# Kernel tuning notes

Hardware: AMD Instinct MI355X
Metric: run time of the kernel (lower is better)

Reference implementation:

```python
import jax, jax.numpy as jnp
import numpy as np

B, L1, L2, D1, D2, H, P = 32, 256, 64, 256, 256, 256, 128
I = D1 + D2  # gate / GRU input dim


def setup_inputs() -> dict:
    key = jax.random.key(0)
    ks = jax.random.split(key, 10)
    s = 0.05  # weight init scale
    return {
        "sequence1": jax.random.normal(ks[0], (B, L1, D1), jnp.float32),
        "sequence2": jax.random.normal(ks[1], (B, L2, D2), jnp.float32),
        "sequence1_mask": jnp.ones((B, L1), jnp.float32),
        "sequence2_mask": jnp.ones((B, L2), jnp.float32),
        "W1": jax.random.normal(ks[2], (D2, P), jnp.float32) * s,
        "W2": jax.random.normal(ks[3], (D1 + H, P), jnp.float32) * s,
        "v": jax.random.normal(ks[4], (P,), jnp.float32) * s,
        "Wg": jax.random.normal(ks[5], (I, I), jnp.float32) * s,
        "bg": jnp.zeros((I,), jnp.float32),
        "w_ih": jax.random.normal(ks[6], (3 * H, I), jnp.float32) * s,
        "w_hh": jax.random.normal(ks[7], (3 * H, H), jnp.float32) * s,
        "b_ih": jnp.zeros((3 * H,), jnp.float32),
        "b_hh": jnp.zeros((3 * H,), jnp.float32),
    }


def reference(sequence1, sequence2, sequence1_mask, sequence2_mask,
              W1, W2, v, Wg, bg, w_ih, w_hh, b_ih, b_hh):
    # Precompute sequence2 projection once: [B, L2, P]
    seq2_proj = jnp.einsum('bld,dp->blp', sequence2, W1)
    # Additive mask for softmax over L2
    neg = jnp.where(sequence2_mask > 0, 0.0, -1e9)  # [B, L2]
    xs = jnp.transpose(sequence1, (1, 0, 2))  # [L1, B, D1]

    def step(h, x_t):
        # attention: v^T tanh(W1*seq2_j + W2*[x_t; h])
        vec = jnp.concatenate([x_t, h], axis=-1)            # [B, D1+H]
        s = jnp.einsum('blp,p->bl',
                       jnp.tanh(seq2_proj + (vec @ W2)[:, None, :]), v) + neg
        w = jax.nn.softmax(s, axis=-1)                      # [B, L2]
        att = jnp.einsum('bl,bld->bd', w, sequence2)        # [B, D2]
        inp = jnp.concatenate([x_t, att], axis=-1)          # [B, I]
        # gated attention: sigmoid(Linear(inp)) * inp
        inp = jax.nn.sigmoid(inp @ Wg.T + bg) * inp
        # GRUCell (torch semantics)
        gi = inp @ w_ih.T + b_ih
        gh = h @ w_hh.T + b_hh
        ir, iz, inn = jnp.split(gi, 3, axis=-1)
        hr, hz, hn = jnp.split(gh, 3, axis=-1)
        r = jax.nn.sigmoid(ir + hr)
        z = jax.nn.sigmoid(iz + hz)
        n = jnp.tanh(inn + r * hn)
        h_new = (1.0 - z) * n + z * h
        return h_new, h_new

    h0 = jnp.zeros((sequence1.shape[0], w_hh.shape[1]), sequence1.dtype)
    _, hs = jax.lax.scan(step, h0, xs)                      # [L1, B, H]
    out = jnp.transpose(hs, (1, 0, 2)) * sequence1_mask[:, :, None]
    return out
```

## Files before the change

### kernel.cpp

```cpp
#include <hip/hip_runtime.h>

typedef _Float16 half2_v __attribute__((ext_vector_type(2)));
typedef unsigned int u32;
typedef unsigned long long u64;

#define W2K_O    0
#define WHHP_O   16384
#define WIHP_O   114688
#define NPACKW   311296
#define S2P_B    1245184
#define S2T_B    1769472
#define M1_B     2818048
#define PROJX_B  4915200
#define GATEX_B  7012352
#define EXCH_B   15400960

#define SMEM_BYTES 149648

__device__ __forceinline__ float fdot2(half2_v a, half2_v b, float c) {
    return __builtin_amdgcn_fdot2(a, b, c, false);
}
__device__ __forceinline__ half2_v h2_of(u32 u) { return __builtin_bit_cast(half2_v, u); }
__device__ __forceinline__ u32 pack_h2(float a, float b) {
    half2_v r; r[0] = (_Float16)a; r[1] = (_Float16)b;
    return __builtin_bit_cast(u32, r);
}
__device__ __forceinline__ float dot4(uint4 w, uint4 a, float acc) {
    acc = fdot2(h2_of(w.x), h2_of(a.x), acc);
    acc = fdot2(h2_of(w.y), h2_of(a.y), acc);
    acc = fdot2(h2_of(w.z), h2_of(a.z), acc);
    acc = fdot2(h2_of(w.w), h2_of(a.w), acc);
    return acc;
}
__device__ __forceinline__ float fast_tanh(float x) {
    float e = __expf(2.0f * x);
    return 1.0f - 2.0f / (e + 1.0f);
}
__device__ __forceinline__ float fast_sigmoid(float x) {
    return 1.0f / (1.0f + __expf(-x));
}
__device__ __forceinline__ u64 aload64(const u64* p) {
    return __hip_atomic_load(p, __ATOMIC_RELAXED, __HIP_MEMORY_SCOPE_AGENT);
}
__device__ __forceinline__ void astore64(u64* p, u64 v) {
    __hip_atomic_store(p, v, __ATOMIC_RELAXED, __HIP_MEMORY_SCOPE_AGENT);
}
__device__ __forceinline__ u32 mkw(float x, u32 st) {
    unsigned short hb = __builtin_bit_cast(unsigned short, (_Float16)x);
    return (st << 16) | (u32)hb;
}
__device__ __forceinline__ u64 mkw64(float a, float b, u32 st) {
    return (u64)mkw(a, st) | ((u64)mkw(b, st) << 32);
}
__device__ __forceinline__ float f16low(u32 v) {
    return (float)__builtin_bit_cast(_Float16, (unsigned short)(v & 0xFFFFu));
}

__global__ void prep_pack_w(const float* __restrict__ W2, const float* __restrict__ wih,
                            const float* __restrict__ whh, u32* __restrict__ ws_u) {
    int idx = blockIdx.x * 256 + threadIdx.x;
    if (idx >= NPACKW) return;
    float a, c;
    if (idx < WHHP_O) {
        int mm = idx >> 11, r = idx & 2047, p = r >> 4, kl = r & 15;
        int row = 256 + mm * 32 + 2 * kl;
        a = W2[row * 128 + p]; c = W2[(row + 1) * 128 + p];
    } else if (idx < WIHP_O) {
        int t2 = idx - WHHP_O, mm = t2 / 12288, r = t2 % 12288, o = r >> 7, k = r & 127;
        int row = (o >> 5) * 256 + mm * 32 + (o & 31);
        a = whh[row * 256 + 2 * k]; c = whh[row * 256 + 2 * k + 1];
    } else {
        int t2 = idx - WIHP_O, mm = t2 / 24576, r = t2 % 24576, o = r >> 8, k = r & 255;
        int row = (o >> 5) * 256 + mm * 32 + (o & 31);
        a = wih[row * 512 + 2 * k]; c = wih[row * 512 + 2 * k + 1];
    }
    ws_u[idx] = pack_h2(a, c);
}

__global__ void prep_s2p(const float* __restrict__ seq2, const float* __restrict__ W1,
                         _Float16* __restrict__ outh) {
    int idx = blockIdx.x * 256 + threadIdx.x;
    int p = idx & 127, j = (idx >> 7) & 63, b = idx >> 13;
    const float* s2 = seq2 + (b * 64 + j) * 256;
    float acc = 0.f;
    #pragma unroll 8
    for (int d = 0; d < 256; ++d) acc += s2[d] * W1[d * 128 + p];
    outh[idx] = (_Float16)acc;
}

__global__ void prep_s2T(const float* __restrict__ seq2, _Float16* __restrict__ dst) {
    int idx = blockIdx.x * 256 + threadIdx.x;
    int j = idx & 63, d = (idx >> 6) & 255, b = idx >> 14;
    dst[idx] = (_Float16)seq2[(b * 64 + j) * 256 + d];
}

__global__ void prep_m1(const float* __restrict__ Wg, const float* __restrict__ seq2,
                        _Float16* __restrict__ dst) {
    int idx = blockIdx.x * 256 + threadIdx.x;
    int j = idx & 63, o = (idx >> 6) & 511, b = idx >> 15;
    const float* wr = Wg + o * 512 + 256;
    const float* s2 = seq2 + (b * 64 + j) * 256;
    float acc = 0.f;
    #pragma unroll 8
    for (int d = 0; d < 256; ++d) acc += wr[d] * s2[d];
    dst[idx] = (_Float16)acc;
}

__global__ void prep_gemm(const float* __restrict__ A, const float* __restrict__ Bsrc,
                          int mode, _Float16* __restrict__ C, int N) {
    __shared__ float As[64][17];
    __shared__ float Bs[16][65];
    int r0 = blockIdx.x * 64, n0 = blockIdx.y * 64;
    int tid = threadIdx.x;
    int tr = tid >> 4, tc = tid & 15;
    float acc[4][4] = {};
    for (int k0 = 0; k0 < 256; k0 += 16) {
        #pragma unroll
        for (int i = 0; i < 4; ++i) {
            int rr = (tid >> 4) + i * 16, kk = tid & 15;
            As[rr][kk] = A[(r0 + rr) * 256 + k0 + kk];
        }
        #pragma unroll
        for (int i = 0; i < 4; ++i) {
            if (mode == 0) { int kk = (tid >> 6) + i * 4, nn = tid & 63; Bs[kk][nn] = Bsrc[(k0 + kk) * N + n0 + nn]; }
            else           { int nn = (tid >> 4) + i * 16, kk = tid & 15; Bs[kk][nn] = Bsrc[(n0 + nn) * 512 + k0 + kk]; }
        }
        __syncthreads();
        #pragma unroll
        for (int k = 0; k < 16; ++k)
            #pragma unroll
            for (int i = 0; i < 4; ++i)
                #pragma unroll
                for (int j = 0; j < 4; ++j)
                    acc[i][j] += As[tr * 4 + i][k] * Bs[k][tc * 4 + j];
        __syncthreads();
    }
    for (int i = 0; i < 4; ++i)
        for (int j = 0; j < 4; ++j)
            C[(size_t)(r0 + tr * 4 + i) * N + n0 + tc * 4 + j] = (_Float16)acc[i][j];
}

__global__ void __launch_bounds__(1024) match_rnn(
    const float* __restrict__ seq1, const float* __restrict__ mask1,
    const float* __restrict__ mask2, const float* __restrict__ v,
    const float* __restrict__ bg, const float* __restrict__ bih,
    const float* __restrict__ bhh, char* __restrict__ ws, float* __restrict__ out)
{
    const int m = blockIdx.x >> 5;
    const int b = blockIdx.x & 31;
    const int tid = threadIdx.x;

    extern __shared__ char smem[];
    u32* s_whh4 = (u32*)smem;
    u32* s_wih4 = s_whh4 + 12288;
    u32* s_w2k  = s_wih4 + 12288;
    u32* s_s2pU = s_w2k + 2176;
    u32* s_m1u  = s_s2pU + 4608;
    u32* s_s2Tu = s_m1u + 2112;
    float* s_redA = (float*)(s_s2Tu + 2112);
    float* s_redD = s_redA + 96;
    u32* s_h2u  = (u32*)(s_redD + 96);
    u32* s_ip2a = s_h2u + 160;
    u32* s_ip2b = s_ip2a + 160;
    float* s_projh = (float*)(s_ip2b + 160);
    float* s_projx = s_projh + 144;
    float* s_v   = s_projx + 144;
    float* s_w   = s_v + 144;
    u32* s_wp   = (u32*)(s_w + 64);
    float* s_neg = (float*)(s_wp + 32);
    float* s_gx  = s_neg + 64;
    float* s_xc  = s_gx + 64;
    float* s_bg  = s_xc + 64;
    float* s_bih = s_bg + 64;
    float* s_bhh = s_bih + 96;
    float* s_hf  = s_bhh + 96;
    u32* s_hloc  = (u32*)(s_hf + 32);
    float* s_m1v = (float*)(s_hloc + 16);

    unsigned short* s_s2p  = (unsigned short*)s_s2pU;

    const u32* wsrc = (const u32*)ws;

    for (int i = tid; i < 12288; i += 1024) {
        int o = i >> 7, k = i & 127, u = k >> 2;
        int du4 = ((o >> 3) * 256) + ((u & 3) * 64) + (((o & 7) << 3) | (u >> 2));
        s_whh4[du4 * 4 + (k & 3)] = wsrc[WHHP_O + m * 12288 + i];
    }
    for (int i = tid; i < 12288; i += 1024) {
        int o = i >> 7, k = i & 127, u = k >> 2;
        int du4 = ((o >> 3) * 256) + ((u & 3) * 64) + (((o & 7) << 3) | (u >> 2));
        s_wih4[du4 * 4 + (k & 3)] = wsrc[WIHP_O + m * 24576 + o * 256 + k];
    }
    for (int i = tid; i < 2048; i += 1024) {
        int p = i >> 4, kl = i & 15;
        s_w2k[p * 17 + kl] = wsrc[W2K_O + m * 2048 + i];
    }
    {
        const u32* s2src = wsrc + (S2P_B / 4) + b * 4096;
        for (int i = tid; i < 4096; i += 1024) {
            int j = i >> 6, kk = i & 63;
            s_s2pU[j * 72 + kk] = s2src[i];
        }
        const u32* m1src = wsrc + (M1_B / 4) + (b * 512 + m * 64) * 32;
        for (int i = tid; i < 2048; i += 1024) {
            int o = i >> 5, jw = i & 31;
            s_m1u[o * 33 + jw] = m1src[i];
        }
        if (m >= 4) {
            const u32* stsrc = wsrc + (S2T_B / 4) + (b * 256 + (m - 4) * 64) * 32;
            for (int i = tid; i < 2048; i += 1024) {
                int dd = i >> 5, jw = i & 31;
                s_s2Tu[dd * 33 + jw] = stsrc[i];
            }
        } else {
            for (int i = tid; i < 2112; i += 1024) s_s2Tu[i] = 0u;
        }
    }
    if (tid < 128) s_v[tid + (tid >> 3)] = v[tid];
    if (tid < 64) { s_neg[tid] = (mask2[b * 64 + tid] > 0.f) ? 0.f : -1e9f; s_bg[tid] = bg[m * 64 + tid]; }
    if (tid < 96) {
        int row = (tid >> 5) * 256 + m * 32 + (tid & 31);
        s_bih[tid] = bih[row]; s_bhh[tid] = bhh[row];
    }
    if (tid < 32) s_hf[tid] = 0.f;

    uint4 wiA = {}, wiB = {}, wiC = {}, wiD = {};
    const int oAD = ((tid >> 6) << 3) + ((tid & 63) >> 3);
    const int ksAD = tid & 7;
    if (tid < 768) {
        const uint4* wip = (const uint4*)(wsrc + WIHP_O + m * 24576 + oAD * 256 + 128 + ksAD * 16);
        wiA = wip[0]; wiB = wip[1]; wiC = wip[2]; wiD = wip[3];
    }

    u64* exch64 = (u64*)(ws + EXCH_B) + (size_t)b * 1024;
    const u32* g_projx = (const u32*)(ws + PROJX_B);
    const u32* g_gatex = (const u32*)(ws + GATEX_B);

    int dead = 0;
    __syncthreads();

    for (int t = 0; t < 256; ++t) {
        const u32 st = (u32)(t + 1);
        float4 xv = {};
        u32 pxv = 0, gxv = 0; float mkv = 0.f;
        if (tid >= 896 && tid < 912) {
            if (m < 4)
                xv = ((const float4*)(seq1 + (size_t)(b * 256 + t) * 256 + m * 64))[tid - 896];
        } else if (tid >= 912 && tid < 976)
            pxv = g_projx[(b * 256 + t) * 64 + (tid - 912)];
        else if (tid >= 976 && tid < 1008)
            gxv = g_gatex[(b * 256 + t) * 256 + m * 32 + (tid - 976)];
        else if (tid == 1008)
            mkv = mask1[b * 256 + t];

        if (t > 0) {
            u64 w1 = 0, w2 = 0;
            const bool q1 = tid < 512, q2 = tid < 128;
            const u32 stp = (u32)t;
            if (!dead) {
                int sp = 0;
                for (;;) {
                    w1 = q1 ? aload64(exch64 + tid) : 0;
                    w2 = q2 ? aload64(exch64 + 512 + tid) : 0;
                    bool ok1 = !q1 || (((((u32)w1) >> 16) == stp) && ((((u32)(w1 >> 32)) >> 16) == stp));
                    bool ok2 = !q2 || (((((u32)w2) >> 16) == stp) && ((((u32)(w2 >> 32)) >> 16) == stp));
                    if (__all((int)(ok1 && ok2))) break;
                    __builtin_amdgcn_s_sleep(1);
                    if (++sp > (1 << 17)) { dead = 1; break; }
                }
            } else {
                w1 = q1 ? aload64(exch64 + tid) : 0;
                w2 = q2 ? aload64(exch64 + 512 + tid) : 0;
            }
            if (q1) {
                float a0 = f16low((u32)w1), a1 = f16low((u32)(w1 >> 32));
                a0 += __shfl_down(a0, 4, 8); a0 += __shfl_down(a0, 2, 8); a0 += __shfl_down(a0, 1, 8);
                a1 += __shfl_down(a1, 4, 8); a1 += __shfl_down(a1, 2, 8); a1 += __shfl_down(a1, 1, 8);
                if ((tid & 7) == 0) {
                    int p0 = (tid >> 3) * 2;
                    int base = p0 + (p0 >> 3);
                    s_projh[base] = a0; s_projh[base + 1] = a1;
                }
            }
            if (q2) {
                u32 val = (((u32)w2) & 0xFFFFu) | ((((u32)(w2 >> 32)) & 0xFFFFu) << 16);
                s_h2u[(tid >> 4) * 20 + (tid & 15)] = val;
            }
        } else {
            if (tid < 160) s_h2u[tid] = 0u;
            if (tid < 144) s_projh[tid] = 0.f;
        }
        if (tid >= 896 && tid < 912) {
            int q = tid - 896;
            s_xc[4 * q] = xv.x; s_xc[4 * q + 1] = xv.y; s_xc[4 * q + 2] = xv.z; s_xc[4 * q + 3] = xv.w;
        } else if (tid >= 912 && tid < 976) {
            half2_v h = h2_of(pxv); int i = tid - 912;
            int base = 2 * i + (i >> 2);
            s_projx[base] = (float)h[0]; s_projx[base + 1] = (float)h[1];
        } else if (tid >= 976 && tid < 1008) {
            half2_v h = h2_of(gxv); int i = tid - 976;
            s_gx[2 * i] = (float)h[0]; s_gx[2 * i + 1] = (float)h[1];
        } else if (tid == 1008) s_m1v[0] = mkv;
        __syncthreads();

        {
            int j = tid >> 4, pk = tid & 15, p0 = pk * 8, pb = pk * 9;
            uint4 sv = *(const uint4*)&s_s2p[j * 144 + p0];
            const u32* su = (const u32*)&sv;
            float acc = 0.f;
            #pragma unroll
            for (int q = 0; q < 4; ++q) {
                half2_v h = h2_of(su[q]);
                int pc = pb + 2 * q;
                float a0 = (float)h[0] + s_projx[pc] + s_projh[pc];
                float a1 = (float)h[1] + s_projx[pc + 1] + s_projh[pc + 1];
                acc += fast_tanh(a0) * s_v[pc];
                acc += fast_tanh(a1) * s_v[pc + 1];
            }
            acc += __shfl_down(acc, 8, 16);
            acc += __shfl_down(acc, 4, 16);
            acc += __shfl_down(acc, 2, 16);
            acc += __shfl_down(acc, 1, 16);
            if (pk == 0) s_w[j] = acc + s_neg[j];
        }
        __syncthreads();
        if (tid < 64) {
            float sc = s_w[tid], mx = sc;
            #pragma unroll
            for (int off = 32; off > 0; off >>= 1) mx = fmaxf(mx, __shfl_xor(mx, off));
            float e = __expf(sc - mx), s = e;
            #pragma unroll
            for (int off = 32; off > 0; off >>= 1) s += __shfl_xor(s, off);
            float wv = e / s;
            float nb = __shfl_down(wv, 1);
            if (!(tid & 1)) s_wp[tid >> 1] = pack_h2(wv, nb);
        }
        __syncthreads();

        if (tid < 512) {
            int o = tid >> 3, r = tid & 7, q = r & 3;
            const u32* src = (r >= 4) ? &s_s2Tu[o * 33] : &s_m1u[o * 33];
            float acc = 0.f;
            #pragma unroll
            for (int c = 0; c < 8; ++c)
                acc = fdot2(h2_of(src[q * 8 + c]), h2_of(s_wp[q * 8 + c]), acc);
            acc += __shfl_down(acc, 2, 4);
            acc += __shfl_down(acc, 1, 4);
            float attv = __shfl_down(acc, 4, 8);
            float fval = 0.f;
            if (r == 0) {
                float g = acc + s_gx[o] + s_bg[o];
                float inpv = (m < 4) ? s_xc[o] : attv;
                fval = fast_sigmoid(g) * inpv;
            }
            float fpn = __shfl_down(fval, 8, 16);
            if ((tid & 15) == 0)
                astore64(&exch64[640 + m * 32 + (tid >> 4)], mkw64(fval, fpn, st));
        }
        if (tid < 768) {
            const uint4* wbase = (const uint4*)s_whh4 + (tid >> 6) * 256;
            float acc = 0.f;
            #pragma unroll
            for (int c = 0; c < 4; ++c) {
                uint4 wv4 = wbase[c * 64 + (tid & 63)];
                uint4 av = *(const uint4*)&s_h2u[ksAD * 20 + c * 4];
                acc = dot4(wv4, av, acc);
            }
            acc += __shfl_down(acc, 4, 8);
            acc += __shfl_down(acc, 2, 8);
            acc += __shfl_down(acc, 1, 8);
            if (ksAD == 0) s_redA[oAD] = acc + s_bhh[oAD];
        }
        if (tid < 256) {
            u64 wv;
            if (!dead) {
                int sp = 0;
                for (;;) {
                    wv = aload64(exch64 + 640 + tid);
                    bool ok = ((((u32)wv) >> 16) == st) && ((((u32)(wv >> 32)) >> 16) == st);
                    if (__all((int)ok)) break;
                    __builtin_amdgcn_s_sleep(1);
                    if (++sp > (1 << 17)) { dead = 1; break; }
                }
            } else wv = aload64(exch64 + 640 + tid);
            u32 val = (((u32)wv) & 0xFFFFu) | ((((u32)(wv >> 32)) & 0xFFFFu) << 16);
            if (tid < 128) s_ip2a[(tid >> 4) * 20 + (tid & 15)] = val;
            else { int j = tid - 128; s_ip2b[(j >> 4) * 20 + (j & 15)] = val; }
        }
        __syncthreads();

        if (tid < 768) {
            const uint4* wbase = (const uint4*)s_wih4 + (tid >> 6) * 256;
            float acc = 0.f;
            #pragma unroll
            for (int c = 0; c < 4; ++c) {
                uint4 wv4 = wbase[c * 64 + (tid & 63)];
                uint4 av = *(const uint4*)&s_ip2a[ksAD * 20 + c * 4];
                acc = dot4(wv4, av, acc);
            }
            acc = dot4(wiA, *(const uint4*)&s_ip2b[ksAD * 20 + 0],  acc);
            acc = dot4(wiB, *(const uint4*)&s_ip2b[ksAD * 20 + 4],  acc);
            acc = dot4(wiC, *(const uint4*)&s_ip2b[ksAD * 20 + 8],  acc);
            acc = dot4(wiD, *(const uint4*)&s_ip2b[ksAD * 20 + 12], acc);
            acc += __shfl_down(acc, 4, 8);
            acc += __shfl_down(acc, 2, 8);
            acc += __shfl_down(acc, 1, 8);
            if (ksAD == 0) s_redD[oAD] = acc + s_bih[oAD];
        }
        __syncthreads();

        if (tid < 32) {
            int o = tid;
            float r_ = fast_sigmoid(s_redD[o] + s_redA[o]);
            float z_ = fast_sigmoid(s_redD[32 + o] + s_redA[32 + o]);
            float n_ = fast_tanh(s_redD[64 + o] + r_ * s_redA[64 + o]);
            float hn = (1.f - z_) * n_ + z_ * s_hf[o];
            s_hf[o] = hn;
            out[(size_t)(b * 256 + t) * 256 + m * 32 + o] = hn * s_m1v[0];
            float nb = __shfl_down(hn, 1);
            if (!(o & 1)) {
                s_hloc[o >> 1] = pack_h2(hn, nb);
                astore64(&exch64[512 + m * 16 + (o >> 1)], mkw64(hn, nb, st));
            }
        }
        __syncthreads();

        if (tid < 512) {
            int p2 = tid >> 3, r = tid & 7;
            int p0 = 2 * p2, u0 = 2 * r;
            float a0 = 0.f, a1 = 0.f;
            #pragma unroll
            for (int cc = 0; cc < 2; ++cc) {
                u32 hp = s_hloc[u0 + cc];
                a0 = fdot2(h2_of(s_w2k[p0 * 17 + u0 + cc]), h2_of(hp), a0);
                a1 = fdot2(h2_of(s_w2k[(p0 + 1) * 17 + u0 + cc]), h2_of(hp), a1);
            }
            a0 += __shfl_down(a0, 4, 8); a0 += __shfl_down(a0, 2, 8); a0 += __shfl_down(a0, 1, 8);
            a1 += __shfl_down(a1, 4, 8); a1 += __shfl_down(a1, 2, 8); a1 += __shfl_down(a1, 1, 8);
            if (r == 0) astore64(&exch64[p2 * 8 + m], mkw64(a0, a1, st));
        }
    }
}

extern "C" void kernel_launch(void* const* d_in, const int* in_sizes, int n_in,
                              void* d_out, int out_size, void* d_ws, size_t ws_size,
                              hipStream_t stream) {
    const float* seq1  = (const float*)d_in[0];
    const float* seq2  = (const float*)d_in[1];
    const float* mask1 = (const float*)d_in[2];
    const float* mask2 = (const float*)d_in[3];
    const float* W1    = (const float*)d_in[4];
    const float* W2    = (const float*)d_in[5];
    const float* v     = (const float*)d_in[6];
    const float* Wg    = (const float*)d_in[7];
    const float* bg    = (const float*)d_in[8];
    const float* wih   = (const float*)d_in[9];
    const float* whh   = (const float*)d_in[10];
    const float* bih   = (const float*)d_in[11];
    const float* bhh   = (const float*)d_in[12];

    char* ws = (char*)d_ws;

    (void)hipFuncSetAttribute(reinterpret_cast<const void*>(match_rnn),
                              hipFuncAttributeMaxDynamicSharedMemorySize, SMEM_BYTES);

    prep_pack_w<<<dim3((NPACKW + 255) / 256), dim3(256), 0, stream>>>(W2, wih, whh, (u32*)ws);
    prep_s2p<<<dim3(1024), dim3(256), 0, stream>>>(seq2, W1, (_Float16*)(ws + S2P_B));
    prep_s2T<<<dim3(2048), dim3(256), 0, stream>>>(seq2, (_Float16*)(ws + S2T_B));
    prep_m1<<<dim3(4096), dim3(256), 0, stream>>>(Wg, seq2, (_Float16*)(ws + M1_B));
    prep_gemm<<<dim3(128, 2), dim3(256), 0, stream>>>(seq1, W2, 0, (_Float16*)(ws + PROJX_B), 128);
    prep_gemm<<<dim3(128, 8), dim3(256), 0, stream>>>(seq1, Wg, 1, (_Float16*)(ws + GATEX_B), 512);
    (void)hipMemsetAsync(ws + EXCH_B, 0, 262144, stream);
    match_rnn<<<dim3(256), dim3(1024), SMEM_BYTES, stream>>>(seq1, mask1, mask2, v, bg, bih, bhh, ws, (float*)d_out);
}
```

Before: 1.524 ms.

## Compute h·W2 projection redundantly per block instead of exchanging partial sums

Each block previously computed a partial of the hidden-state projection through W2 for its slice of h, published the partials through global memory, and consumers reduced them. Now every block holds the full W2 hidden slice in registers and recomputes the whole projection locally from the exchanged h. This removes the 512-entry partial-sum exchange, a __syncthreads, and the post-GRU projection phase from the critical path. The cost is redundant FMA work in every block plus an extra barrier after the projection.

```diff
diff --git a/kernel.cpp b/kernel.cpp
--- a/kernel.cpp
+++ b/kernel.cpp
@@ -15,7 +15,7 @@
 #define GATEX_B  7012352
 #define EXCH_B   15400960
 
-#define SMEM_BYTES 149648
+#define SMEM_BYTES 140368
 
 __device__ __forceinline__ float fdot2(half2_v a, half2_v b, float c) {
     return __builtin_amdgcn_fdot2(a, b, c, false);
@@ -62,8 +62,8 @@
     if (idx >= NPACKW) return;
     float a, c;
     if (idx < WHHP_O) {
-        int mm = idx >> 11, r = idx & 2047, p = r >> 4, kl = r & 15;
-        int row = 256 + mm * 32 + 2 * kl;
+        int p = idx >> 7, kp = idx & 127;
+        int row = 256 + 2 * kp;
         a = W2[row * 128 + p]; c = W2[(row + 1) * 128 + p];
     } else if (idx < WIHP_O) {
         int t2 = idx - WHHP_O, mm = t2 / 12288, r = t2 % 12288, o = r >> 7, k = r & 127;
@@ -153,8 +153,7 @@
     extern __shared__ char smem[];
     u32* s_whh4 = (u32*)smem;
     u32* s_wih4 = s_whh4 + 12288;
-    u32* s_w2k  = s_wih4 + 12288;
-    u32* s_s2pU = s_w2k + 2176;
+    u32* s_s2pU = s_wih4 + 12288;
     u32* s_m1u  = s_s2pU + 4608;
     u32* s_s2Tu = s_m1u + 2112;
     float* s_redA = (float*)(s_s2Tu + 2112);
@@ -174,8 +173,7 @@
     float* s_bih = s_bg + 64;
     float* s_bhh = s_bih + 96;
     float* s_hf  = s_bhh + 96;
-    u32* s_hloc  = (u32*)(s_hf + 32);
-    float* s_m1v = (float*)(s_hloc + 16);
+    float* s_m1v = s_hf + 32;
 
     unsigned short* s_s2p  = (unsigned short*)s_s2pU;
 
@@ -190,10 +188,6 @@
         int o = i >> 7, k = i & 127, u = k >> 2;
         int du4 = ((o >> 3) * 256) + ((u & 3) * 64) + (((o & 7) << 3) | (u >> 2));
         s_wih4[du4 * 4 + (k & 3)] = wsrc[WIHP_O + m * 24576 + o * 256 + k];
-    }
-    for (int i = tid; i < 2048; i += 1024) {
-        int p = i >> 4, kl = i & 15;
-        s_w2k[p * 17 + kl] = wsrc[W2K_O + m * 2048 + i];
     }
     {
         const u32* s2src = wsrc + (S2P_B / 4) + b * 4096;
@@ -230,6 +224,11 @@
     if (tid < 768) {
         const uint4* wip = (const uint4*)(wsrc + WIHP_O + m * 24576 + oAD * 256 + 128 + ksAD * 16);
         wiA = wip[0]; wiB = wip[1]; wiC = wip[2]; wiD = wip[3];
+    }
+    uint4 w2A, w2B, w2C, w2D;
+    {
+        const uint4* wp2 = (const uint4*)(wsrc + W2K_O + (tid >> 3) * 128 + (tid & 7) * 16);
+        w2A = wp2[0]; w2B = wp2[1]; w2C = wp2[2]; w2D = wp2[3];
     }
 
     u64* exch64 = (u64*)(ws + EXCH_B) + (size_t)b * 1024;
@@ -254,41 +253,25 @@
             mkv = mask1[b * 256 + t];
 
         if (t > 0) {
-            u64 w1 = 0, w2 = 0;
-            const bool q1 = tid < 512, q2 = tid < 128;
+            u64 w2v = 0;
+            const bool q2 = tid < 128;
             const u32 stp = (u32)t;
             if (!dead) {
                 int sp = 0;
                 for (;;) {
-                    w1 = q1 ? aload64(exch64 + tid) : 0;
-                    w2 = q2 ? aload64(exch64 + 512 + tid) : 0;
-                    bool ok1 = !q1 || (((((u32)w1) >> 16) == stp) && ((((u32)(w1 >> 32)) >> 16) == stp));
-                    bool ok2 = !q2 || (((((u32)w2) >> 16) == stp) && ((((u32)(w2 >> 32)) >> 16) == stp));
-                    if (__all((int)(ok1 && ok2))) break;
+                    w2v = q2 ? aload64(exch64 + tid) : 0;
+                    bool ok2 = !q2 || (((((u32)w2v) >> 16) == stp) && ((((u32)(w2v >> 32)) >> 16) == stp));
+                    if (__all((int)ok2)) break;
                     __builtin_amdgcn_s_sleep(1);
                     if (++sp > (1 << 17)) { dead = 1; break; }
                 }
-            } else {
-                w1 = q1 ? aload64(exch64 + tid) : 0;
-                w2 = q2 ? aload64(exch64 + 512 + tid) : 0;
-            }
-            if (q1) {
-                float a0 = f16low((u32)w1), a1 = f16low((u32)(w1 >> 32));
-                a0 += __shfl_down(a0, 4, 8); a0 += __shfl_down(a0, 2, 8); a0 += __shfl_down(a0, 1, 8);
-                a1 += __shfl_down(a1, 4, 8); a1 += __shfl_down(a1, 2, 8); a1 += __shfl_down(a1, 1, 8);
-                if ((tid & 7) == 0) {
-                    int p0 = (tid >> 3) * 2;
-                    int base = p0 + (p0 >> 3);
-                    s_projh[base] = a0; s_projh[base + 1] = a1;
-                }
-            }
+            } else w2v = q2 ? aload64(exch64 + tid) : 0;
             if (q2) {
-                u32 val = (((u32)w2) & 0xFFFFu) | ((((u32)(w2 >> 32)) & 0xFFFFu) << 16);
+                u32 val = (((u32)w2v) & 0xFFFFu) | ((((u32)(w2v >> 32)) & 0xFFFFu) << 16);
                 s_h2u[(tid >> 4) * 20 + (tid & 15)] = val;
             }
         } else {
             if (tid < 160) s_h2u[tid] = 0u;
-            if (tid < 144) s_projh[tid] = 0.f;
         }
         if (tid >= 896 && tid < 912) {
             int q = tid - 896;
@@ -304,6 +287,21 @@
         __syncthreads();
 
         {
+            int p = tid >> 3, kg = tid & 7;
+            const u32* hb = &s_h2u[kg * 20];
+            float a = 0.f;
+            a = dot4(w2A, *(const uint4*)&hb[0],  a);
+            a = dot4(w2B, *(const uint4*)&hb[4],  a);
+            a = dot4(w2C, *(const uint4*)&hb[8],  a);
+            a = dot4(w2D, *(const uint4*)&hb[12], a);
+            a += __shfl_down(a, 4, 8);
+            a += __shfl_down(a, 2, 8);
+            a += __shfl_down(a, 1, 8);
+            if (kg == 0) s_projh[p + (p >> 3)] = a;
+        }
+        __syncthreads();
+
+        {
             int j = tid >> 4, pk = tid & 15, p0 = pk * 8, pb = pk * 9;
             uint4 sv = *(const uint4*)&s_s2p[j * 144 + p0];
             const u32* su = (const u32*)&sv;
@@ -355,7 +353,7 @@
             }
             float fpn = __shfl_down(fval, 8, 16);
             if ((tid & 15) == 0)
-                astore64(&exch64[640 + m * 32 + (tid >> 4)], mkw64(fval, fpn, st));
+                astore64(&exch64[128 + m * 32 + (tid >> 4)], mkw64(fval, fpn, st));
         }
         if (tid < 768) {
             const uint4* wbase = (const uint4*)s_whh4 + (tid >> 6) * 256;
@@ -376,13 +374,13 @@
             if (!dead) {
                 int sp = 0;
                 for (;;) {
-                    wv = aload64(exch64 + 640 + tid);
+                    wv = aload64(exch64 + 128 + tid);
                     bool ok = ((((u32)wv) >> 16) == st) && ((((u32)(wv >> 32)) >> 16) == st);
                     if (__all((int)ok)) break;
                     __builtin_amdgcn_s_sleep(1);
                     if (++sp > (1 << 17)) { dead = 1; break; }
                 }
-            } else wv = aload64(exch64 + 640 + tid);
+            } else wv = aload64(exch64 + 128 + tid);
             u32 val = (((u32)wv) & 0xFFFFu) | ((((u32)(wv >> 32)) & 0xFFFFu) << 16);
             if (tid < 128) s_ip2a[(tid >> 4) * 20 + (tid & 15)] = val;
             else { int j = tid - 128; s_ip2b[(j >> 4) * 20 + (j & 15)] = val; }
@@ -418,26 +416,7 @@
             s_hf[o] = hn;
             out[(size_t)(b * 256 + t) * 256 + m * 32 + o] = hn * s_m1v[0];
             float nb = __shfl_down(hn, 1);
-            if (!(o & 1)) {
-                s_hloc[o >> 1] = pack_h2(hn, nb);
-                astore64(&exch64[512 + m * 16 + (o >> 1)], mkw64(hn, nb, st));
-            }
-        }
-        __syncthreads();
-
-        if (tid < 512) {
-            int p2 = tid >> 3, r = tid & 7;
-            int p0 = 2 * p2, u0 = 2 * r;
-            float a0 = 0.f, a1 = 0.f;
-            #pragma unroll
-            for (int cc = 0; cc < 2; ++cc) {
-                u32 hp = s_hloc[u0 + cc];
-                a0 = fdot2(h2_of(s_w2k[p0 * 17 + u0 + cc]), h2_of(hp), a0);
-                a1 = fdot2(h2_of(s_w2k[(p0 + 1) * 17 + u0 + cc]), h2_of(hp), a1);
-            }
-            a0 += __shfl_down(a0, 4, 8); a0 += __shfl_down(a0, 2, 8); a0 += __shfl_down(a0, 1, 8);
-            a1 += __shfl_down(a1, 4, 8); a1 += __shfl_down(a1, 2, 8); a1 += __shfl_down(a1, 1, 8);
-            if (r == 0) astore64(&exch64[p2 * 8 + m], mkw64(a0, a1, st));
+            if (!(o & 1)) astore64(&exch64[m * 16 + (o >> 1)], mkw64(hn, nb, st));
         }
     }
 }
```

Result: no change. 1.534 ms (+0.7%).
